# Kernel tuning notes

Measured on AMD Instinct MI355X. Metric: run time of the kernel, lower is better.

Reference implementation:

```python
import jax, jax.numpy as jnp
import numpy as np

N = 200000      # nodes
E = 1600000     # directed edges (before self-loops)
G = 5000        # graphs (molecules)
IN, HID, OUT, HEADS = 128, 128, 128, 3


def gat_layer(x, src, dst, W, a_src, a_dst, b, heads, out_dim, concat):
    n = x.shape[0]
    h = (x @ W).reshape(n, heads, out_dim)                 # [N,H,F]
    al_s = jnp.einsum('nhf,hf->nh', h, a_src)              # [N,H]
    al_d = jnp.einsum('nhf,hf->nh', h, a_dst)
    e = jax.nn.leaky_relu(al_s[src] + al_d[dst], 0.2)      # [E,H]
    m = jax.ops.segment_max(e, dst, num_segments=n)        # softmax over incoming edges
    ex = jnp.exp(e - m[dst])
    den = jax.ops.segment_sum(ex, dst, num_segments=n)
    alpha = ex / (den[dst] + 1e-16)                        # [E,H]
    msg = h[src] * alpha[..., None]                        # [E,H,F]
    agg = jax.ops.segment_sum(msg, dst, num_segments=n)    # [N,H,F]
    agg = agg.reshape(n, heads * out_dim) if concat else agg.mean(axis=1)
    return agg + b


def setup_inputs() -> dict:
    key = jax.random.key(0)
    ks = jax.random.split(key, 16)
    d = {}
    d['x'] = jax.random.normal(ks[0], (N, IN), dtype=jnp.float32)
    d['edge_index'] = jax.random.randint(ks[1], (2, E), 0, N, dtype=jnp.int64)
    d['batch'] = jnp.sort(jax.random.randint(ks[2], (N,), 0, G, dtype=jnp.int64))
    s = 0.1
    d['W1'] = jax.random.normal(ks[3], (IN, HEADS * HID), jnp.float32) * s
    d['a1s'] = jax.random.normal(ks[4], (HEADS, HID), jnp.float32) * s
    d['a1d'] = jax.random.normal(ks[5], (HEADS, HID), jnp.float32) * s
    d['b1'] = jnp.zeros((HEADS * HID,), jnp.float32)
    d['W2'] = jax.random.normal(ks[6], (HEADS * HID, HEADS * HID), jnp.float32) * s
    d['a2s'] = jax.random.normal(ks[7], (HEADS, HID), jnp.float32) * s
    d['a2d'] = jax.random.normal(ks[8], (HEADS, HID), jnp.float32) * s
    d['b2'] = jnp.zeros((HEADS * HID,), jnp.float32)
    d['W3'] = jax.random.normal(ks[9], (HEADS * HID, OUT), jnp.float32) * s
    d['a3s'] = jax.random.normal(ks[10], (1, OUT), jnp.float32) * s
    d['a3d'] = jax.random.normal(ks[11], (1, OUT), jnp.float32) * s
    d['b3'] = jnp.zeros((OUT,), jnp.float32)
    return d


def reference(x, edge_index, batch, W1, a1s, a1d, b1, W2, a2s, a2d, b2, W3, a3s, a3d, b3):
    # PyG GATConv default add_self_loops=True
    loops = jnp.arange(N, dtype=edge_index.dtype)
    src = jnp.concatenate([edge_index[0], loops])
    dst = jnp.concatenate([edge_index[1], loops])
    h = jax.nn.leaky_relu(gat_layer(x, src, dst, W1, a1s, a1d, b1, HEADS, HID, True), 0.2)
    h = jax.nn.leaky_relu(gat_layer(h, src, dst, W2, a2s, a2d, b2, HEADS, HID, True), 0.2)
    h = jax.nn.leaky_relu(gat_layer(h, src, dst, W3, a3s, a3d, b3, 1, OUT, False), 0.2)
    # global mean pool over graphs
    sums = jax.ops.segment_sum(h, batch, num_segments=G)            # [G,OUT]
    cnt = jax.ops.segment_sum(jnp.ones((N,), h.dtype), batch, num_segments=G)
    return sums / jnp.maximum(cnt, 1.0)[:, None]
```

## Files before the change

kernel.cpp:

```cpp
#include <hip/hip_runtime.h>
#include <hip/hip_bf16.h>
#include <math.h>

#define LRELU_SLOPE 0.2f
typedef __hip_bfloat16 bf16;
typedef __hip_bfloat162 bf16x2;

typedef short s8v __attribute__((ext_vector_type(8)));
typedef float f4v __attribute__((ext_vector_type(4)));

__device__ __forceinline__ float lrelu(float v) { return v > 0.f ? v : LRELU_SLOPE * v; }
__device__ __forceinline__ float b2f(short b) {
  return __uint_as_float(((unsigned)(unsigned short)b) << 16);
}

__device__ __forceinline__ void st2(bf16* p, float x, float y) {
  float2 f{x, y};
  *(bf16x2*)p = __float22bfloat162_rn(f);
}
__device__ __forceinline__ void st2(float* p, float x, float y) {
  *(float2*)p = float2{x, y};
}

__device__ __forceinline__ void st2_nt(bf16* p, float x, float y) {
  float2 f{x, y};
  bf16x2 v = __float22bfloat162_rn(f);
  __builtin_nontemporal_store(*(unsigned int*)&v, (unsigned int*)p);
}
__device__ __forceinline__ void st2_nt(float* p, float x, float y) {
  __builtin_nontemporal_store(x, p);
  __builtin_nontemporal_store(y, p + 1);
}


__global__ void k_zero(unsigned int* __restrict__ p, long n) {
  long i = (long)blockIdx.x * blockDim.x + threadIdx.x;
  if (i < n) p[i] = 0u;
}

__global__ void k_zero_out(float* __restrict__ out, int n) {
  int i = blockIdx.x * blockDim.x + threadIdx.x;
  if (i < n) out[i] = 0.f;
}


__global__ void k_cvt(const float* __restrict__ x, bf16* __restrict__ xb, long n) {
  long i = (long)blockIdx.x * blockDim.x + threadIdx.x;
  if (i < n) xb[i] = __float2bfloat16(x[i]);
}

__global__ void k_tw(const float* __restrict__ W, bf16* __restrict__ Wt, int K, int NN) {
  int i = blockIdx.x * blockDim.x + threadIdx.x;
  if (i >= K * NN) return;
  int k = i / NN, n = i - k * NN;
  Wt[(size_t)n * K + k] = __float2bfloat16(W[i]);
}


__global__ void k_hist(const int* __restrict__ dst, int* __restrict__ deg, int E, int Et) {
  int e = blockIdx.x * blockDim.x + threadIdx.x;
  if (e >= Et) return;
  int d = (e < E) ? dst[e] : (e - E);
  atomicAdd(&deg[d], 1);
}

__global__ void k_hist1(const int* __restrict__ idx, int* __restrict__ deg, int n) {
  int i = blockIdx.x * blockDim.x + threadIdx.x;
  if (i < n) atomicAdd(&deg[idx[i]], 1);
}

__global__ void k_scan1(const int* __restrict__ deg, int* __restrict__ offs,
                        int* __restrict__ bsum, int n) {
  __shared__ int sd[256];
  int t = threadIdx.x;
  int base = blockIdx.x * 1024 + t * 4;
  int v[4]; int tsum = 0;
#pragma unroll
  for (int i = 0; i < 4; ++i) { v[i] = (base + i < n) ? deg[base + i] : 0; tsum += v[i]; }
  sd[t] = tsum;
  __syncthreads();
  for (int off = 1; off < 256; off <<= 1) {
    int x = (t >= off) ? sd[t - off] : 0;
    __syncthreads();
    sd[t] += x;
    __syncthreads();
  }
  int excl = sd[t] - tsum;
#pragma unroll
  for (int i = 0; i < 4; ++i) { if (base + i < n) offs[base + i] = excl; excl += v[i]; }
  if (t == 255) bsum[blockIdx.x] = sd[255];
}

__global__ void k_scan2(int* bsum, int nb) {
  if (threadIdx.x == 0 && blockIdx.x == 0) {
    int run = 0;
    for (int i = 0; i < nb; ++i) { int t = bsum[i]; bsum[i] = run; run += t; }
  }
}

__global__ void k_scan3(int* __restrict__ offs, const int* __restrict__ bsum, int n, int total) {
  int t = threadIdx.x;
  int base = blockIdx.x * 1024 + t * 4;
  int add = bsum[blockIdx.x];
#pragma unroll
  for (int i = 0; i < 4; ++i) if (base + i < n) offs[base + i] += add;
  if (blockIdx.x == 0 && t == 0) offs[n] = total;
}

__global__ void k_scatter(const int* __restrict__ src, const int* __restrict__ dst,
                          const int* __restrict__ offs, int* __restrict__ cur,
                          int* __restrict__ ssrc, int E, int Et) {
  int e = blockIdx.x * blockDim.x + threadIdx.x;
  if (e >= Et) return;
  int s, d;
  if (e < E) { s = src[e]; d = dst[e]; } else { s = d = e - E; }
  int pos = offs[d] + atomicAdd(&cur[d], 1);
  ssrc[pos] = s;
}


__global__ __launch_bounds__(256) void k_gemm_mfma(const bf16* __restrict__ A,
                                                   const bf16* __restrict__ Wt,
                                                   bf16* __restrict__ C,
                                                   int K, int NN) {
  __shared__ __align__(16) short sA[64 * 64];
  int t = threadIdx.x;
  int wv = t >> 6, lane = t & 63;
  int quad = lane >> 4, l15 = lane & 15;
  size_t bm0 = (size_t)blockIdx.x * 64;
  int bn0 = blockIdx.y * 64;
  const bf16* Ab = A + bm0 * K;
  const bf16* Bp = Wt + (size_t)(bn0 + wv * 16 + l15) * K;
  f4v acc[4] = {f4v{0,0,0,0}, f4v{0,0,0,0}, f4v{0,0,0,0}, f4v{0,0,0,0}};

  for (int kb = 0; kb < K; kb += 64) {
#pragma unroll
    for (int j = 0; j < 2; ++j) {
      int idx = j * 256 + t;
      int row = idx >> 3, p = idx & 7;
      int c = p ^ (row & 7);
      const bf16* g = Ab + (size_t)row * K + kb + c * 8;
      __builtin_amdgcn_global_load_lds(
          (const __attribute__((address_space(1))) void*)g,
          (__attribute__((address_space(3))) void*)((char*)sA + (size_t)(j * 256 + wv * 64) * 16),
          16, 0, 0);
    }
    __syncthreads();
#pragma unroll
    for (int kk = 0; kk < 2; ++kk) {
      s8v bfrag = *(const s8v*)(Bp + kb + kk * 32 + quad * 8);
#pragma unroll
      for (int ms = 0; ms < 4; ++ms) {
        int row = ms * 16 + l15;
        int pos = (kk * 4 + quad) ^ (row & 7);
        s8v afrag = *(const s8v*)((const char*)sA + (size_t)row * 128 + pos * 16);
        acc[ms] = __builtin_amdgcn_mfma_f32_16x16x32_bf16(afrag, bfrag, acc[ms], 0, 0, 0);
      }
    }
    __syncthreads();
  }
  int coln = bn0 + wv * 16 + l15;
#pragma unroll
  for (int ms = 0; ms < 4; ++ms)
#pragma unroll
    for (int r = 0; r < 4; ++r)
      C[(bm0 + ms * 16 + quad * 4 + r) * NN + coln] = __float2bfloat16(acc[ms][r]);
}


template <int H>
__global__ void k_al(const bf16* __restrict__ h, const float* __restrict__ as,
                     const float* __restrict__ ad, float* __restrict__ al_s,
                     float* __restrict__ al_d, int N) {
  int n = (blockIdx.x * blockDim.x + threadIdx.x) >> 6;
  int lane = threadIdx.x & 63;
  if (n >= N) return;
  int hd = lane >> 4;
  bool active = (hd < H);
  int hdc = active ? hd : 0;
  int f8 = (lane & 15) * 8;
  const bf16* hp = h + (size_t)n * (H * 128) + hdc * 128 + f8;
  s8v hv = *(const s8v*)hp;
  float ss = 0.f, sd = 0.f;
#pragma unroll
  for (int i = 0; i < 8; ++i) {
    float v = b2f(hv[i]);
    ss += v * as[hdc * 128 + f8 + i];
    sd += v * ad[hdc * 128 + f8 + i];
  }
#pragma unroll
  for (int off = 8; off; off >>= 1) {
    ss += __shfl_xor(ss, off, 64);
    sd += __shfl_xor(sd, off, 64);
  }
  if (active && (lane & 15) == 0) {
    al_s[n * H + hd] = ss;
    al_d[n * H + hd] = sd;
  }
}


template <int H, typename OT>
__global__ __launch_bounds__(256) void k_attn_agg(const bf16* __restrict__ hbuf,
                           const int* __restrict__ ssrc,
                           const int* __restrict__ offs, const float* __restrict__ al_s,
                           const float* __restrict__ al_d, const float* __restrict__ bias,
                           OT* __restrict__ out, int N) {
  constexpr int SW = (H > 1) ? 4 : 2;
  __shared__ __align__(16) float stash[4][64 * SW];
  int n = (blockIdx.x * blockDim.x + threadIdx.x) >> 6;
  int lane = threadIdx.x & 63;
  if (n >= N) return;
  float* st = stash[threadIdx.x >> 6];
  int start = offs[n], end = offs[n + 1];
  float ald[H], mx[H];
#pragma unroll
  for (int hd = 0; hd < H; ++hd) { ald[hd] = al_d[n * H + hd]; mx[hd] = -1e30f; }

  for (int pos = start + lane; pos < end; pos += 64) {
    int s = ssrc[pos];
#pragma unroll
    for (int hd = 0; hd < H; ++hd)
      mx[hd] = fmaxf(mx[hd], lrelu(al_s[s * H + hd] + ald[hd]));
  }
#pragma unroll
  for (int hd = 0; hd < H; ++hd)
#pragma unroll
    for (int off = 32; off; off >>= 1) mx[hd] = fmaxf(mx[hd], __shfl_xor(mx[hd], off, 64));

  int f0 = lane * 2;
  float den[H], accx[H], accy[H];
#pragma unroll
  for (int hd = 0; hd < H; ++hd) { den[hd] = 0.f; accx[hd] = 0.f; accy[hd] = 0.f; }

  for (int cb = start; cb < end; cb += 64) {
    int cl = end - cb; if (cl > 64) cl = 64;
    int mys = (lane < cl) ? ssrc[cb + lane] : 0;
    float myex[H];
#pragma unroll
    for (int hd = 0; hd < H; ++hd) {
      float e = lrelu(al_s[mys * H + hd] + ald[hd]);
      float ex = __expf(e - mx[hd]);
      myex[hd] = (lane < cl) ? ex : 0.f;
    }
    __builtin_amdgcn_wave_barrier();
    if (H > 1) {
      float4 s4{__int_as_float(mys), myex[0], myex[1], myex[2]};
      *(float4*)&st[lane * 4] = s4;
    } else {
      float2 s2{__int_as_float(mys), myex[0]};
      *(float2*)&st[lane * 2] = s2;
    }
    asm volatile("s_waitcnt lgkmcnt(0)" ::: "memory");
    __builtin_amdgcn_wave_barrier();

    for (int r = 0; r < cl; r += 8) {
      int su[8];
      float a[8][H];
#pragma unroll
      for (int u = 0; u < 8; ++u) {
        if (H > 1) {
          float4 ed = *(const float4*)&st[(r + u) * 4];
          su[u] = __float_as_int(ed.x);
          a[u][0] = ed.y;
          if (H > 1) { a[u][1] = ed.z; a[u][2] = ed.w; }
        } else {
          float2 ed = *(const float2*)&st[(r + u) * 2];
          su[u] = __float_as_int(ed.x);
          a[u][0] = ed.y;
        }
      }
      bf16x2 v[8][H];
#pragma unroll
      for (int u = 0; u < 8; ++u) {
        const bf16* hp = hbuf + (size_t)su[u] * (H * 128) + f0;
#pragma unroll
        for (int hd = 0; hd < H; ++hd) v[u][hd] = *(const bf16x2*)(hp + hd * 128);
      }
#pragma unroll
      for (int u = 0; u < 8; ++u)
#pragma unroll
        for (int hd = 0; hd < H; ++hd) {
          float2 f = __bfloat1622float2(v[u][hd]);
          accx[hd] += a[u][hd] * f.x;
          accy[hd] += a[u][hd] * f.y;
          if (hd == 0) {}
        }
#pragma unroll
      for (int u = 0; u < 8; ++u)
#pragma unroll
        for (int hd = 0; hd < H; ++hd) den[hd] += a[u][hd];
    }
  }
#pragma unroll
  for (int hd = 0; hd < H; ++hd) {
    float r = 1.f / (den[hd] + 1e-16f);
    float ox = lrelu(accx[hd] * r + bias[hd * 128 + f0]);
    float oy = lrelu(accy[hd] * r + bias[hd * 128 + f0 + 1]);
    st2_nt(&out[((size_t)n * H + hd) * 128 + f0], ox, oy);
  }
}


__global__ void k_pool(const float* __restrict__ h, const int* __restrict__ goffs,
                       float* __restrict__ out, int G) {
  int g = (blockIdx.x * blockDim.x + threadIdx.x) >> 6;
  int lane = threadIdx.x & 63;
  if (g >= G) return;
  int s = goffs[g], e = goffs[g + 1];
  float ax = 0.f, ay = 0.f;
  for (int n = s; n < e; ++n) {
    float2 v = *(const float2*)&h[(size_t)n * 128 + lane * 2];
    ax += v.x; ay += v.y;
  }
  float c = fmaxf((float)(e - s), 1.f);
  st2(&out[(size_t)g * 128 + lane * 2], ax / c, ay / c);
}


extern "C" void kernel_launch(void* const* d_in, const int* in_sizes, int n_in,
                              void* d_out, int out_size, void* d_ws, size_t ws_size,
                              hipStream_t stream) {
  const float* x   = (const float*)d_in[0];
  const int*   ei  = (const int*)d_in[1];
  const int*   bat = (const int*)d_in[2];
  const float* W1  = (const float*)d_in[3];
  const float* a1s = (const float*)d_in[4];
  const float* a1d = (const float*)d_in[5];
  const float* b1  = (const float*)d_in[6];
  const float* W2  = (const float*)d_in[7];
  const float* a2s = (const float*)d_in[8];
  const float* a2d = (const float*)d_in[9];
  const float* b2  = (const float*)d_in[10];
  const float* W3  = (const float*)d_in[11];
  const float* a3s = (const float*)d_in[12];
  const float* a3d = (const float*)d_in[13];
  const float* b3  = (const float*)d_in[14];
  float* out = (float*)d_out;

  const int N = in_sizes[2];
  const int E = in_sizes[1] / 2;
  const int Et = E + N;
  const int G = out_size / 128;

  char* p = (char*)d_ws;
  auto carve = [&](size_t bytes) { void* r = (void*)p; p += (bytes + 255) & ~(size_t)255; return r; };
  bf16*  bufA   = (bf16*)carve((size_t)N * 384 * 2);
  bf16*  bufB   = (bf16*)carve((size_t)N * 384 * 2);
  float* al_s   = (float*)carve((size_t)N * 3 * 4);
  float* al_d   = (float*)carve((size_t)N * 3 * 4);
  int*   ssrc   = (int*)carve((size_t)Et * 4);
  int*   offs   = (int*)carve((size_t)(N + 1) * 4);
  int*   deg    = (int*)carve((size_t)N * 4);
  int*   cur    = (int*)carve((size_t)N * 4);
  int*   bsum   = (int*)carve(4096 * 4);
  int*   gdeg   = (int*)carve((size_t)G * 4);
  int*   goffs  = (int*)carve((size_t)(G + 1) * 4);
  bf16*  Wt1    = (bf16*)carve((size_t)384 * 128 * 2);
  bf16*  Wt2    = (bf16*)carve((size_t)384 * 384 * 2);
  bf16*  Wt3    = (bf16*)carve((size_t)128 * 384 * 2);
  size_t need = (size_t)(p - (char*)d_ws);

  if (ws_size < need) {
    k_zero_out<<<(out_size + 255) / 256, 256, 0, stream>>>(out, out_size);
    return;
  }

  const int* esrc = ei;
  const int* edst = ei + E;

  int ebl = (Et + 255) / 256;
  int NB = (N + 1023) / 1024;
  int GB = (G + 1023) / 1024;
  int nodeWaveBlocks = (N * 64 + 255) / 256;

  bf16* xb = bufA;
  k_cvt<<<((long)N * 128 + 255) / 256, 256, 0, stream>>>(x, xb, (long)N * 128);
  k_tw<<<(128 * 384 + 255) / 256, 256, 0, stream>>>(W1, Wt1, 128, 384);
  k_tw<<<(384 * 384 + 255) / 256, 256, 0, stream>>>(W2, Wt2, 384, 384);
  k_tw<<<(384 * 128 + 255) / 256, 256, 0, stream>>>(W3, Wt3, 384, 128);

  k_zero<<<(N + 255) / 256, 256, 0, stream>>>((unsigned int*)deg, N);
  k_hist<<<ebl, 256, 0, stream>>>(edst, deg, E, Et);
  k_scan1<<<NB, 256, 0, stream>>>(deg, offs, bsum, N);
  k_scan2<<<1, 64, 0, stream>>>(bsum, NB);
  k_scan3<<<NB, 256, 0, stream>>>(offs, bsum, N, Et);
  k_zero<<<(N + 255) / 256, 256, 0, stream>>>((unsigned int*)cur, N);
  k_scatter<<<ebl, 256, 0, stream>>>(esrc, edst, offs, cur, ssrc, E, Et);

  k_zero<<<(G + 255) / 256, 256, 0, stream>>>((unsigned int*)gdeg, G);
  k_hist1<<<(N + 255) / 256, 256, 0, stream>>>(bat, gdeg, N);
  k_scan1<<<GB, 256, 0, stream>>>(gdeg, goffs, bsum, G);
  k_scan2<<<1, 64, 0, stream>>>(bsum, GB);
  k_scan3<<<GB, 256, 0, stream>>>(goffs, bsum, G, N);

  dim3 g1(N / 64, 6), g2(N / 64, 6), g3(N / 64, 2);

  k_gemm_mfma<<<g1, 256, 0, stream>>>(xb, Wt1, bufB, 128, 384);
  k_al<3><<<nodeWaveBlocks, 256, 0, stream>>>(bufB, a1s, a1d, al_s, al_d, N);
  k_attn_agg<3, bf16><<<nodeWaveBlocks, 256, 0, stream>>>(bufB, ssrc, offs, al_s, al_d, b1, bufA, N);

  k_gemm_mfma<<<g2, 256, 0, stream>>>(bufA, Wt2, bufB, 384, 384);
  k_al<3><<<nodeWaveBlocks, 256, 0, stream>>>(bufB, a2s, a2d, al_s, al_d, N);
  k_attn_agg<3, bf16><<<nodeWaveBlocks, 256, 0, stream>>>(bufB, ssrc, offs, al_s, al_d, b2, bufA, N);

  k_gemm_mfma<<<g3, 256, 0, stream>>>(bufA, Wt3, bufB, 384, 128);
  k_al<1><<<nodeWaveBlocks, 256, 0, stream>>>(bufB, a3s, a3d, al_s, al_d, N);
  float* out3 = (float*)bufA;
  k_attn_agg<1, float><<<nodeWaveBlocks, 256, 0, stream>>>(bufB, ssrc, offs, al_s, al_d, b3, out3, N);

  k_pool<<<(G * 64 + 255) / 256, 256, 0, stream>>>(out3, goffs, out, G);
}
```

Measured before the change: 1.474 ms.

## Use online softmax and wide per-lane gathers in GAT aggregation

```diff
diff --git a/kernel.cpp b/kernel.cpp
--- a/kernel.cpp
+++ b/kernel.cpp
@@ -7,6 +7,7 @@
 typedef __hip_bfloat162 bf16x2;
 
 typedef short s8v __attribute__((ext_vector_type(8)));
+typedef short s4v __attribute__((ext_vector_type(4)));
 typedef float f4v __attribute__((ext_vector_type(4)));
 
 __device__ __forceinline__ float lrelu(float v) { return v > 0.f ? v : LRELU_SLOPE * v; }
@@ -14,22 +15,16 @@
   return __uint_as_float(((unsigned)(unsigned short)b) << 16);
 }
 
-__device__ __forceinline__ void st2(bf16* p, float x, float y) {
-  float2 f{x, y};
-  *(bf16x2*)p = __float22bfloat162_rn(f);
-}
 __device__ __forceinline__ void st2(float* p, float x, float y) {
   *(float2*)p = float2{x, y};
 }
 
-__device__ __forceinline__ void st2_nt(bf16* p, float x, float y) {
-  float2 f{x, y};
-  bf16x2 v = __float22bfloat162_rn(f);
-  __builtin_nontemporal_store(*(unsigned int*)&v, (unsigned int*)p);
-}
-__device__ __forceinline__ void st2_nt(float* p, float x, float y) {
-  __builtin_nontemporal_store(x, p);
-  __builtin_nontemporal_store(y, p + 1);
+template <typename T>
+__device__ __forceinline__ void nt_store16(void* p, T v) {
+  union { T t; unsigned long long q[2]; } u;
+  u.t = v;
+  __builtin_nontemporal_store(u.q[0], (unsigned long long*)p);
+  __builtin_nontemporal_store(u.q[1], (unsigned long long*)p + 1);
 }
 
 
@@ -172,6 +167,7 @@
 __global__ void k_al(const bf16* __restrict__ h, const float* __restrict__ as,
                      const float* __restrict__ ad, float* __restrict__ al_s,
                      float* __restrict__ al_d, int N) {
+  constexpr int SP = (H > 1) ? 4 : 1;
   int n = (blockIdx.x * blockDim.x + threadIdx.x) >> 6;
   int lane = threadIdx.x & 63;
   if (n >= N) return;
@@ -194,11 +190,15 @@
     sd += __shfl_xor(sd, off, 64);
   }
   if (active && (lane & 15) == 0) {
-    al_s[n * H + hd] = ss;
-    al_d[n * H + hd] = sd;
-  }
-}
-
+    al_s[n * SP + hd] = ss;
+    al_d[n * SP + hd] = sd;
+  }
+}
+
+
+template <int CPL> struct HVec;
+template <> struct HVec<8> { typedef s8v T; };
+template <> struct HVec<4> { typedef s4v T; };
 
 template <int H, typename OT>
 __global__ __launch_bounds__(256) void k_attn_agg(const bf16* __restrict__ hbuf,
@@ -206,45 +206,80 @@
                            const int* __restrict__ offs, const float* __restrict__ al_s,
                            const float* __restrict__ al_d, const float* __restrict__ bias,
                            OT* __restrict__ out, int N) {
-  constexpr int SW = (H > 1) ? 4 : 2;
+  constexpr int SW  = (H > 1) ? 4 : 2;
+  constexpr int ROW = H * 128;
+  constexpr int CPL = (H > 1) ? 8 : 4;
+  constexpr int NL  = ROW / CPL;
+  typedef typename HVec<CPL>::T hvec;
+
   __shared__ __align__(16) float stash[4][64 * SW];
   int n = (blockIdx.x * blockDim.x + threadIdx.x) >> 6;
   int lane = threadIdx.x & 63;
   if (n >= N) return;
   float* st = stash[threadIdx.x >> 6];
   int start = offs[n], end = offs[n + 1];
-  float ald[H], mx[H];
-#pragma unroll
-  for (int hd = 0; hd < H; ++hd) { ald[hd] = al_d[n * H + hd]; mx[hd] = -1e30f; }
-
-  for (int pos = start + lane; pos < end; pos += 64) {
-    int s = ssrc[pos];
-#pragma unroll
-    for (int hd = 0; hd < H; ++hd)
-      mx[hd] = fmaxf(mx[hd], lrelu(al_s[s * H + hd] + ald[hd]));
-  }
-#pragma unroll
-  for (int hd = 0; hd < H; ++hd)
-#pragma unroll
-    for (int off = 32; off; off >>= 1) mx[hd] = fmaxf(mx[hd], __shfl_xor(mx[hd], off, 64));
-
-  int f0 = lane * 2;
-  float den[H], accx[H], accy[H];
-#pragma unroll
-  for (int hd = 0; hd < H; ++hd) { den[hd] = 0.f; accx[hd] = 0.f; accy[hd] = 0.f; }
+
+  float ald[H];
+  if constexpr (H > 1) {
+    float4 t = *(const float4*)&al_d[(size_t)n * 4];
+    ald[0] = t.x; ald[1] = t.y; ald[2] = t.z;
+  } else {
+    ald[0] = al_d[n];
+  }
+
+  bool act = lane < NL;
+  int c0 = act ? lane * CPL : 0;
+  int hd_l = c0 >> 7;
+
+  float m[H];
+  float den = 0.f;
+  float acc[CPL];
+#pragma unroll
+  for (int hd = 0; hd < H; ++hd) m[hd] = -1e30f;
+#pragma unroll
+  for (int i = 0; i < CPL; ++i) acc[i] = 0.f;
 
   for (int cb = start; cb < end; cb += 64) {
     int cl = end - cb; if (cl > 64) cl = 64;
-    int mys = (lane < cl) ? ssrc[cb + lane] : 0;
+    bool el = lane < cl;
+    int mys = el ? ssrc[cb + lane] : 0;
+    float ev[H];
+    if constexpr (H > 1) {
+      float4 av = *(const float4*)&al_s[(size_t)mys * 4];
+      ev[0] = av.x; ev[1] = av.y; ev[2] = av.z;
+    } else {
+      ev[0] = al_s[mys];
+    }
+#pragma unroll
+    for (int hd = 0; hd < H; ++hd)
+      ev[hd] = el ? lrelu(ev[hd] + ald[hd]) : -1e30f;
+
+    float nm[H];
+#pragma unroll
+    for (int hd = 0; hd < H; ++hd) {
+      float v = ev[hd];
+#pragma unroll
+      for (int off = 32; off; off >>= 1) v = fmaxf(v, __shfl_xor(v, off, 64));
+      nm[hd] = fmaxf(v, m[hd]);
+    }
+    if (cb > start) {
+      float sc[H];
+#pragma unroll
+      for (int hd = 0; hd < H; ++hd) sc[hd] = __expf(m[hd] - nm[hd]);
+      float so = sc[hd_l];
+      den *= so;
+#pragma unroll
+      for (int i = 0; i < CPL; ++i) acc[i] *= so;
+    }
+#pragma unroll
+    for (int hd = 0; hd < H; ++hd) m[hd] = nm[hd];
+
     float myex[H];
 #pragma unroll
-    for (int hd = 0; hd < H; ++hd) {
-      float e = lrelu(al_s[mys * H + hd] + ald[hd]);
-      float ex = __expf(e - mx[hd]);
-      myex[hd] = (lane < cl) ? ex : 0.f;
-    }
+    for (int hd = 0; hd < H; ++hd) myex[hd] = el ? __expf(ev[hd] - m[hd]) : 0.f;
+
     __builtin_amdgcn_wave_barrier();
-    if (H > 1) {
+    if constexpr (H > 1) {
       float4 s4{__int_as_float(mys), myex[0], myex[1], myex[2]};
       *(float4*)&st[lane * 4] = s4;
     } else {
@@ -255,49 +290,52 @@
     __builtin_amdgcn_wave_barrier();
 
     for (int r = 0; r < cl; r += 8) {
-      int su[8];
-      float a[8][H];
+      int su[8]; float a[8];
 #pragma unroll
       for (int u = 0; u < 8; ++u) {
-        if (H > 1) {
+        if constexpr (H > 1) {
           float4 ed = *(const float4*)&st[(r + u) * 4];
           su[u] = __float_as_int(ed.x);
-          a[u][0] = ed.y;
-          if (H > 1) { a[u][1] = ed.z; a[u][2] = ed.w; }
+          a[u] = (hd_l == 0) ? ed.y : ((hd_l == 1) ? ed.z : ed.w);
         } else {
           float2 ed = *(const float2*)&st[(r + u) * 2];
           su[u] = __float_as_int(ed.x);
-          a[u][0] = ed.y;
+          a[u] = ed.y;
         }
+        den += a[u];
       }
-      bf16x2 v[8][H];
-#pragma unroll
-      for (int u = 0; u < 8; ++u) {
-        const bf16* hp = hbuf + (size_t)su[u] * (H * 128) + f0;
-#pragma unroll
-        for (int hd = 0; hd < H; ++hd) v[u][hd] = *(const bf16x2*)(hp + hd * 128);
+      hvec hv[8];
+#pragma unroll
+      for (int u = 0; u < 8; ++u)
+        hv[u] = *(const hvec*)(hbuf + (size_t)su[u] * ROW + c0);
+#pragma unroll
+      for (int u = 0; u < 8; ++u)
+#pragma unroll
+        for (int i = 0; i < CPL; ++i)
+          acc[i] += a[u] * b2f(hv[u][i]);
+    }
+  }
+
+  if (act) {
+    float rr = 1.f / (den + 1e-16f);
+    OT* op = out + (size_t)n * ROW + c0;
+    if constexpr (sizeof(OT) == 2) {
+      s8v ov;
+#pragma unroll
+      for (int i = 0; i < CPL; ++i) {
+        float o = lrelu(acc[i] * rr + bias[c0 + i]);
+        bf16 b = __float2bfloat16(o);
+        ov[i] = *(short*)&b;
       }
-#pragma unroll
-      for (int u = 0; u < 8; ++u)
-#pragma unroll
-        for (int hd = 0; hd < H; ++hd) {
-          float2 f = __bfloat1622float2(v[u][hd]);
-          accx[hd] += a[u][hd] * f.x;
-          accy[hd] += a[u][hd] * f.y;
-          if (hd == 0) {}
-        }
-#pragma unroll
-      for (int u = 0; u < 8; ++u)
-#pragma unroll
-        for (int hd = 0; hd < H; ++hd) den[hd] += a[u][hd];
-    }
-  }
-#pragma unroll
-  for (int hd = 0; hd < H; ++hd) {
-    float r = 1.f / (den[hd] + 1e-16f);
-    float ox = lrelu(accx[hd] * r + bias[hd * 128 + f0]);
-    float oy = lrelu(accy[hd] * r + bias[hd * 128 + f0 + 1]);
-    st2_nt(&out[((size_t)n * H + hd) * 128 + f0], ox, oy);
+      nt_store16(op, ov);
+    } else {
+      float4 ov;
+      ov.x = lrelu(acc[0] * rr + bias[c0 + 0]);
+      ov.y = lrelu(acc[1] * rr + bias[c0 + 1]);
+      ov.z = lrelu(acc[2] * rr + bias[c0 + 2]);
+      ov.w = lrelu(acc[3] * rr + bias[c0 + 3]);
+      nt_store16(op, ov);
+    }
   }
 }
 
@@ -347,8 +385,8 @@
   auto carve = [&](size_t bytes) { void* r = (void*)p; p += (bytes + 255) & ~(size_t)255; return r; };
   bf16*  bufA   = (bf16*)carve((size_t)N * 384 * 2);
   bf16*  bufB   = (bf16*)carve((size_t)N * 384 * 2);
-  float* al_s   = (float*)carve((size_t)N * 3 * 4);
-  float* al_d   = (float*)carve((size_t)N * 3 * 4);
+  float* al_s   = (float*)carve((size_t)N * 4 * 4);
+  float* al_d   = (float*)carve((size_t)N * 4 * 4);
   int*   ssrc   = (int*)carve((size_t)Et * 4);
   int*   offs   = (int*)carve((size_t)(N + 1) * 4);
   int*   deg    = (int*)carve((size_t)N * 4);
```

After: 1.508 ms. 1.02x slower.
